# Optimization experiments

Hardware: AMD Instinct MI355X
Metric: run time of the kernel (lower is better)

Reference implementation:

```python
import jax, jax.numpy as jnp
import numpy as np

M, K, N, G = 64, 4096, 11008, 128  # tokens, infeatures, outfeatures, group_size
NUM_GROUPS = K // G  # 32


def _fp8_round_trip(w):
    # Simulate FP8 E4M3 storage of the quantized weight codes.
    return w.astype(jnp.float8_e4m3fn).astype(jnp.float32)


def setup_inputs() -> dict:
    key = jax.random.key(0)
    k1, k2, k3, k4 = jax.random.split(key, 4)
    x = jax.random.normal(k1, (M, K), dtype=jnp.float32)
    # FP8-representable weight codes (post round-trip, stored as f32 values)
    weight = _fp8_round_trip(jax.random.normal(k2, (N, K), dtype=jnp.float32) * 2.0)
    # Per-(out_feature, group) dequant scales, strictly positive
    weight_scale = jax.random.uniform(k3, (N, NUM_GROUPS), dtype=jnp.float32,
                                      minval=0.005, maxval=0.02)
    bias = jax.random.normal(k4, (N,), dtype=jnp.float32)
    return {"x": x, "weight": weight, "weight_scale": weight_scale, "bias": bias}


def reference(x, weight, weight_scale, bias):
    # Dequantize: each group of `G` consecutive in-features of an output row
    # shares one scale -> w_deq[o, i] = weight[o, i] * scale[o, i // G]
    n, k = weight.shape
    g = k // weight_scale.shape[1]
    w_deq = (weight.reshape(n, -1, g) * weight_scale[:, :, None]).reshape(n, k)
    # Fused dequant-matmul: out[m, o] = sum_i x[m, i] * w_deq[o, i] + bias[o]
    out = jnp.einsum("mk,nk->mn", x, w_deq) + bias
    return out
```

## Files before the change

### kernel.cpp

```cpp
#include <hip/hip_runtime.h>


#define Md 64
#define Kd 4096
#define Nd 11008
#define NGROUPS 32
#define BN 64
#define KSPLIT 8
#define KCHUNK (Kd / KSPLIT)
#define NST (KCHUNK / 32)
#define NGRP (KCHUNK / 128)

typedef __attribute__((ext_vector_type(8))) __bf16 bf16x8;
typedef __attribute__((ext_vector_type(4))) float f32x4;

#define AS1 __attribute__((address_space(1)))
#define AS3 __attribute__((address_space(3)))

__global__ __launch_bounds__(256)
void prep(const float* __restrict__ x, __bf16* __restrict__ xf,
          const float* __restrict__ bias, float* __restrict__ out)
{
    if (blockIdx.x < 128) {
        const int tid  = blockIdx.x * 256 + threadIdx.x;
        const int lane = tid & 63;
        const int t    = (tid >> 6) & 3;
        const int kb   = tid >> 8;
        const int row  = t * 16 + (lane & 15);
        const int col  = kb * 32 + (lane >> 4) * 8;
        const float4 a = *(const float4*)(x + (size_t)row * Kd + col);
        const float4 b = *(const float4*)(x + (size_t)row * Kd + col + 4);
        bf16x8 v = {(__bf16)a.x, (__bf16)a.y, (__bf16)a.z, (__bf16)a.w,
                    (__bf16)b.x, (__bf16)b.y, (__bf16)b.z, (__bf16)b.w};
        *(bf16x8*)(xf + (size_t)tid * 8) = v;
    } else {
        const int i4 = (blockIdx.x - 128) * 256 + threadIdx.x;
        const int n  = (i4 * 4) % Nd;
        *(float4*)(out + (size_t)i4 * 4) = *(const float4*)(bias + n);
    }
}

__global__ __launch_bounds__(256, 4)
void qlinear_pass1(const float* __restrict__ w,
                   const __bf16* __restrict__ xf,
                   const float* __restrict__ scale,
                   float* __restrict__ out)
{
    const int tid  = threadIdx.x;
    const int wv   = tid >> 6;
    const int lane = tid & 63;
    const int quad = lane >> 4;
    const int ln   = lane & 15;

    const int n0 = blockIdx.x * BN;
    const int ky = blockIdx.y;
    const int k0 = ky * KCHUNK;

    __shared__ alignas(16) float  lds_w[3][BN * 32];
    __shared__ alignas(16) __bf16 lds_x[3][2048];

    const float* src[2];
    #pragma unroll
    for (int j = 0; j < 2; ++j) {
        const int r   = wv * 16 + j * 8 + (lane >> 3);
        const int c16 = (lane & 7) ^ (r & 7);
        src[j] = w + (size_t)(n0 + r) * Kd + k0 + c16 * 4;
    }

    const __bf16* xq = xf + ((size_t)ky * 64 + wv) * 512 + (size_t)lane * 8;

#define STAGE(S, B)                                                            \
    do {                                                                       \
        _Pragma("unroll")                                                      \
        for (int j = 0; j < 2; ++j)                                            \
            __builtin_amdgcn_global_load_lds(                                  \
                (const AS1 void*)(src[j] + (S) * 32),                          \
                (AS3 void*)&lds_w[B][(wv * 16 + j * 8) * 32], 16, 0, 0);       \
        __builtin_amdgcn_global_load_lds(                                      \
            (const AS1 void*)(xq + (size_t)(S) * 2048),                        \
            (AS3 void*)&lds_x[B][wv * 512], 16, 0, 0);                         \
    } while (0)

    const int nrow = n0 + wv * 16 + ln;
    float4 sc4 = *(const float4*)(scale + (size_t)nrow * NGROUPS + ky * NGRP);
    asm volatile("s_waitcnt vmcnt(0)" ::: "memory");
    const float sc[4] = {sc4.x, sc4.y, sc4.z, sc4.w};

    const int rr = wv * 16 + ln;
    const int rx = rr & 7;

    f32x4 acc[4];
    #pragma unroll
    for (int t = 0; t < 4; ++t) acc[t] = (f32x4){0.f, 0.f, 0.f, 0.f};

    STAGE(0, 0);
    STAGE(1, 1);
    asm volatile("s_waitcnt vmcnt(3)" ::: "memory");
    __builtin_amdgcn_s_barrier();

    #pragma unroll
    for (int g = 0; g < NGRP; ++g) {
        f32x4 pg[4];
        #pragma unroll
        for (int t = 0; t < 4; ++t) pg[t] = (f32x4){0.f, 0.f, 0.f, 0.f};

        #pragma unroll
        for (int sub = 0; sub < 4; ++sub) {
            const int s   = g * 4 + sub;
            const int buf = s % 3;

            if (s + 2 < NST) STAGE(s + 2, (s + 2) % 3);

            bf16x8 xv[4];
            #pragma unroll
            for (int t = 0; t < 4; ++t)
                xv[t] = *(const bf16x8*)&lds_x[buf][t * 512 + lane * 8];

            const int cA = (quad * 2) ^ rx;
            const int cB = (quad * 2 + 1) ^ rx;
            f32x4 fa = *(const f32x4*)&lds_w[buf][rr * 32 + cA * 4];
            f32x4 fb = *(const f32x4*)&lds_w[buf][rr * 32 + cB * 4];
            bf16x8 wf = {(__bf16)fa.x, (__bf16)fa.y, (__bf16)fa.z, (__bf16)fa.w,
                         (__bf16)fb.x, (__bf16)fb.y, (__bf16)fb.z, (__bf16)fb.w};

            #pragma unroll
            for (int t = 0; t < 4; ++t)
                pg[t] = __builtin_amdgcn_mfma_f32_16x16x32_bf16(xv[t], wf, pg[t],
                                                                0, 0, 0);

            if (s + 1 < NST) {
                if (s + 2 < NST)
                    asm volatile("s_waitcnt vmcnt(3)" ::: "memory");
                else
                    asm volatile("s_waitcnt vmcnt(0)" ::: "memory");
                __builtin_amdgcn_s_barrier();
            }
        }

        const float s = sc[g];
        #pragma unroll
        for (int t = 0; t < 4; ++t)
            #pragma unroll
            for (int r = 0; r < 4; ++r)
                acc[t][r] += s * pg[t][r];
    }

    float* op = out + n0 + wv * 16 + ln;
    #pragma unroll
    for (int t = 0; t < 4; ++t)
        #pragma unroll
        for (int r = 0; r < 4; ++r)
            unsafeAtomicAdd(&op[(size_t)(t * 16 + quad * 4 + r) * Nd], acc[t][r]);
#undef STAGE
}

extern "C" void kernel_launch(void* const* d_in, const int* in_sizes, int n_in,
                              void* d_out, int out_size, void* d_ws, size_t ws_size,
                              hipStream_t stream) {
    const float* x     = (const float*)d_in[0];
    const float* w     = (const float*)d_in[1];
    const float* scale = (const float*)d_in[2];
    const float* bias  = (const float*)d_in[3];
    float* out = (float*)d_out;
    float* ws  = (float*)d_ws;

    __bf16* xf = (__bf16*)ws;

    prep<<<816, 256, 0, stream>>>(x, xf, bias, out);

    dim3 grid1(Nd / BN, KSPLIT);
    qlinear_pass1<<<grid1, 256, 0, stream>>>(w, xf, scale, out);
}
```

Measured before the change: 273.6 us.

## Deepen weight prefetch to 5 LDS buffers, stream x into registers, drop barriers

Activation tiles are now loaded straight from global memory into registers per wave instead of being shared through LDS. The fp32 weight tiles use a 5-buffer LDS ring with prefetch distance 4. Each wave only reads LDS rows it loaded itself, so the workgroup barriers are replaced by per-wave vmcnt waits, which removes the cross-wave synchronisation cost. The trade-offs are four times the x reads from L2 (each wave fetches all four row tiles), more registers, and a drop in the occupancy hint from 4 to 3 blocks per CU.

```diff
diff --git a/kernel.cpp b/kernel.cpp
--- a/kernel.cpp
+++ b/kernel.cpp
@@ -9,7 +9,8 @@
 #define KSPLIT 8
 #define KCHUNK (Kd / KSPLIT)
 #define NST (KCHUNK / 32)
-#define NGRP (KCHUNK / 128)
+#define NBUF 5
+#define DIST 4
 
 typedef __attribute__((ext_vector_type(8))) __bf16 bf16x8;
 typedef __attribute__((ext_vector_type(4))) float f32x4;
@@ -40,7 +41,7 @@
     }
 }
 
-__global__ __launch_bounds__(256, 4)
+__global__ __launch_bounds__(256, 3)
 void qlinear_pass1(const float* __restrict__ w,
                    const __bf16* __restrict__ xf,
                    const float* __restrict__ scale,
@@ -56,8 +57,7 @@
     const int ky = blockIdx.y;
     const int k0 = ky * KCHUNK;
 
-    __shared__ alignas(16) float  lds_w[3][BN * 32];
-    __shared__ alignas(16) __bf16 lds_x[3][2048];
+    __shared__ alignas(16) float lds_w[NBUF][BN * 32];
 
     const float* src[2];
     #pragma unroll
@@ -67,82 +67,82 @@
         src[j] = w + (size_t)(n0 + r) * Kd + k0 + c16 * 4;
     }
 
-    const __bf16* xq = xf + ((size_t)ky * 64 + wv) * 512 + (size_t)lane * 8;
-
-#define STAGE(S, B)                                                            \
+#define WSTAGE(S, B)                                                           \
     do {                                                                       \
         _Pragma("unroll")                                                      \
-        for (int j = 0; j < 2; ++j)                                            \
+        for (int j = 0; j < 2; ++j)                                           \
             __builtin_amdgcn_global_load_lds(                                  \
                 (const AS1 void*)(src[j] + (S) * 32),                          \
                 (AS3 void*)&lds_w[B][(wv * 16 + j * 8) * 32], 16, 0, 0);       \
-        __builtin_amdgcn_global_load_lds(                                      \
-            (const AS1 void*)(xq + (size_t)(S) * 2048),                        \
-            (AS3 void*)&lds_x[B][wv * 512], 16, 0, 0);                         \
+    } while (0)
+
+    const __bf16* xp = xf + (size_t)ky * NST * 4 * 512 + (size_t)lane * 8;
+    bf16x8 xr[4][4];
+
+#define XLOAD(SLOT, S)                                                         \
+    do {                                                                       \
+        _Pragma("unroll")                                                      \
+        for (int t = 0; t < 4; ++t)                                           \
+            xr[SLOT][t] = *(const bf16x8*)(xp + ((size_t)(S) * 4 + t) * 512);  \
     } while (0)
 
     const int nrow = n0 + wv * 16 + ln;
-    float4 sc4 = *(const float4*)(scale + (size_t)nrow * NGROUPS + ky * NGRP);
+    float4 sc4 = *(const float4*)(scale + (size_t)nrow * NGROUPS + ky * 4);
     asm volatile("s_waitcnt vmcnt(0)" ::: "memory");
     const float sc[4] = {sc4.x, sc4.y, sc4.z, sc4.w};
 
     const int rr = wv * 16 + ln;
     const int rx = rr & 7;
 
-    f32x4 acc[4];
+    f32x4 acc[4], pg[4];
     #pragma unroll
-    for (int t = 0; t < 4; ++t) acc[t] = (f32x4){0.f, 0.f, 0.f, 0.f};
+    for (int t = 0; t < 4; ++t) {
+        acc[t] = (f32x4){0.f, 0.f, 0.f, 0.f};
+        pg[t]  = (f32x4){0.f, 0.f, 0.f, 0.f};
+    }
 
-    STAGE(0, 0);
-    STAGE(1, 1);
-    asm volatile("s_waitcnt vmcnt(3)" ::: "memory");
-    __builtin_amdgcn_s_barrier();
+    WSTAGE(0, 0); XLOAD(0, 0);
+    WSTAGE(1, 1); XLOAD(1, 1);
+    WSTAGE(2, 2); XLOAD(2, 2);
+    WSTAGE(3, 3); XLOAD(3, 3);
 
     #pragma unroll
-    for (int g = 0; g < NGRP; ++g) {
-        f32x4 pg[4];
-        #pragma unroll
-        for (int t = 0; t < 4; ++t) pg[t] = (f32x4){0.f, 0.f, 0.f, 0.f};
+    for (int s = 0; s < NST; ++s) {
+        if (s + DIST < NST) WSTAGE(s + DIST, (s + DIST) % NBUF);
+
+        if (s + DIST < NST)      asm volatile("s_waitcnt vmcnt(20)" ::: "memory");
+        else if (s == NST - 4)   asm volatile("s_waitcnt vmcnt(18)" ::: "memory");
+        else if (s == NST - 3)   asm volatile("s_waitcnt vmcnt(12)" ::: "memory");
+        else if (s == NST - 2)   asm volatile("s_waitcnt vmcnt(6)"  ::: "memory");
+        else                     asm volatile("s_waitcnt vmcnt(0)"  ::: "memory");
+        __builtin_amdgcn_sched_barrier(0);
+
+        const int buf = s % NBUF;
+        const int cA  = (quad * 2) ^ rx;
+        const int cB  = (quad * 2 + 1) ^ rx;
+        f32x4 fa = *(const f32x4*)&lds_w[buf][rr * 32 + cA * 4];
+        f32x4 fb = *(const f32x4*)&lds_w[buf][rr * 32 + cB * 4];
+        bf16x8 wf = {(__bf16)fa.x, (__bf16)fa.y, (__bf16)fa.z, (__bf16)fa.w,
+                     (__bf16)fb.x, (__bf16)fb.y, (__bf16)fb.z, (__bf16)fb.w};
 
         #pragma unroll
-        for (int sub = 0; sub < 4; ++sub) {
-            const int s   = g * 4 + sub;
-            const int buf = s % 3;
+        for (int t = 0; t < 4; ++t)
+            pg[t] = __builtin_amdgcn_mfma_f32_16x16x32_bf16(xr[s & 3][t], wf,
+                                                            pg[t], 0, 0, 0);
 
-            if (s + 2 < NST) STAGE(s + 2, (s + 2) % 3);
+        if (s + DIST < NST) XLOAD(s & 3, s + DIST);
 
-            bf16x8 xv[4];
+        if ((s & 3) == 3) {
+            const float sg = sc[s >> 2];
             #pragma unroll
-            for (int t = 0; t < 4; ++t)
-                xv[t] = *(const bf16x8*)&lds_x[buf][t * 512 + lane * 8];
-
-            const int cA = (quad * 2) ^ rx;
-            const int cB = (quad * 2 + 1) ^ rx;
-            f32x4 fa = *(const f32x4*)&lds_w[buf][rr * 32 + cA * 4];
-            f32x4 fb = *(const f32x4*)&lds_w[buf][rr * 32 + cB * 4];
-            bf16x8 wf = {(__bf16)fa.x, (__bf16)fa.y, (__bf16)fa.z, (__bf16)fa.w,
-                         (__bf16)fb.x, (__bf16)fb.y, (__bf16)fb.z, (__bf16)fb.w};
-
-            #pragma unroll
-            for (int t = 0; t < 4; ++t)
-                pg[t] = __builtin_amdgcn_mfma_f32_16x16x32_bf16(xv[t], wf, pg[t],
-                                                                0, 0, 0);
-
-            if (s + 1 < NST) {
-                if (s + 2 < NST)
-                    asm volatile("s_waitcnt vmcnt(3)" ::: "memory");
-                else
-                    asm volatile("s_waitcnt vmcnt(0)" ::: "memory");
-                __builtin_amdgcn_s_barrier();
+            for (int t = 0; t < 4; ++t) {
+                #pragma unroll
+                for (int r = 0; r < 4; ++r) {
+                    acc[t][r] += sg * pg[t][r];
+                    pg[t][r] = 0.f;
+                }
             }
         }
-
-        const float s = sc[g];
-        #pragma unroll
-        for (int t = 0; t < 4; ++t)
-            #pragma unroll
-            for (int r = 0; r < 4; ++r)
-                acc[t][r] += s * pg[t][r];
     }
 
     float* op = out + n0 + wv * 16 + ln;
@@ -151,7 +151,8 @@
         #pragma unroll
         for (int r = 0; r < 4; ++r)
             unsafeAtomicAdd(&op[(size_t)(t * 16 + quad * 4 + r) * Nd], acc[t][r]);
-#undef STAGE
+#undef WSTAGE
+#undef XLOAD
 }
 
 extern "C" void kernel_launch(void* const* d_in, const int* in_sizes, int n_in,
```

New measurement: 267.4 us (median of 2 runs). 2.2% less time.
